# Kernel tuning notes

Measured on AMD Instinct MI355X. Metric: run time of the kernel, lower is better.

Reference implementation:

```python
import jax, jax.numpy as jnp
import numpy as np
import math

B, T, N, D = 8, 4, 2048, 256
M, E = 4096, 8

def setup_inputs() -> dict:
    key = jax.random.key(0)
    ks = jax.random.split(key, 8)
    std = 0.02
    return {
        "prop_embed": jax.random.normal(ks[0], (B, T, N, D), jnp.float32),
        "adap_embed": jax.random.normal(ks[1], (B, N, D), jnp.float32),
        "x_proj_w": jax.random.normal(ks[2], (D, D), jnp.float32) * (1.0 / np.sqrt(D)),
        "x_proj_b": jnp.zeros((D,), jnp.float32),
        "keyMatrix": jax.random.normal(ks[3], (M, D), jnp.float32) * std,
        "memMatrix": jax.random.normal(ks[4], (M, D), jnp.float32) * std,
        "w_gate": jax.random.normal(ks[5], (D, E), jnp.float32) * (1.0 / np.sqrt(D)),
        "w_noise": jax.random.normal(ks[6], (D, E), jnp.float32) * (1.0 / np.sqrt(D)),
    }

def reference(prop_embed, adap_embed, x_proj_w, x_proj_b, keyMatrix, memMatrix, w_gate, w_noise):
    b, t, n, d = prop_embed.shape
    m = memMatrix.shape[0]
    x = jnp.mean(prop_embed, axis=1)                      # [B,N,D]
    q = jnp.tanh(x @ x_proj_w.T + x_proj_b)               # [B,N,D]
    att = jnp.einsum('bnd,md->bnm', q, keyMatrix)         # [B,N,M]
    # eval mode: noise_stddev * self.training == 0, so noisy_logits == clean_logits
    clean_logits = memMatrix @ w_gate                     # [M,E]
    mem_label = jax.nn.softmax(clean_logits, axis=-1)     # [M,E]
    # sparse_qk: keep top-k = int(ln(M)) logits, rest -> -inf
    k = int(math.log(m))
    vals, idx = jax.lax.top_k(att, k)                     # [B,N,k]
    att2 = jnp.full((b * n, m), -jnp.inf, dtype=att.dtype)
    rows = jnp.arange(b * n)[:, None]
    att2 = att2.at[rows, idx.reshape(b * n, k)].set(vals.reshape(b * n, k))
    att_w = jax.nn.softmax(att2, axis=-1).reshape(b, n, m)
    mem_retrieved = jnp.einsum('bnm,md->bnd', att_w, memMatrix)
    label_retrieved = jnp.einsum('bnm,me->bne', att_w, mem_label)
    gate = label_retrieved
    return (gate, mem_retrieved, label_retrieved, mem_label, att_w)
```

## Files before the change

kernel.cpp:

```cpp
#include <hip/hip_runtime.h>
#include <hip/hip_fp16.h>
#include <math.h>

#define Bb 8
#define Tt 4
#define Nn 2048
#define Dd 256
#define Mm 4096
#define Ee 8
#define ROWS (Bb*Nn)
#define KSEL 8
#define KC 16

#define O_GATE 0LL
#define O_MEMR 131072LL
#define O_LABR 4325376LL
#define O_MLAB 4456448LL
#define O_ATTW 4489216LL

#define WS_WT    0LL
#define WS_KH    262144LL
#define WS_CAND  16777216LL
#define WS_QH    150994944LL

typedef float f32x4 __attribute__((ext_vector_type(4)));
typedef short short8 __attribute__((ext_vector_type(8)));
typedef _Float16 f16x8 __attribute__((ext_vector_type(8)));

__device__ __forceinline__ unsigned short f2h(float x) {
    __half h = __float2half(x);
    return *reinterpret_cast<unsigned short*>(&h);
}

__device__ __forceinline__ void gload_lds16(const void* g, void* l) {
    __builtin_amdgcn_global_load_lds(
        (const __attribute__((address_space(1))) unsigned int*)g,
        (__attribute__((address_space(3))) unsigned int*)l,
        16, 0, 0);
}

__global__ __launch_bounds__(256) void k_prep(const float* __restrict__ W, float* __restrict__ WT,
                                              const float* __restrict__ key, unsigned short* __restrict__ kh,
                                              const float* __restrict__ mem, const float* __restrict__ wg,
                                              float* __restrict__ mlab) {
    int b = blockIdx.x, tid = threadIdx.x;
    if (b < 256) {
        int i = b * 256 + tid;
        int r = i >> 8, c = i & 255;
        WT[c * 256 + r] = W[r * 256 + c];
    } else if (b < 256 + 4096) {
        int idx = (b - 256) * 256 + tid;
        kh[idx] = f2h(key[idx]);
    } else {
        int m = (b - 4352) * 256 + tid;
        if (m < Mm) {
            float acc[Ee];
            #pragma unroll
            for (int e = 0; e < Ee; ++e) acc[e] = 0.f;
            const float* mr = mem + (long long)m * Dd;
            for (int d = 0; d < Dd; ++d) {
                float mv = mr[d];
                #pragma unroll
                for (int e = 0; e < Ee; ++e) acc[e] = fmaf(mv, wg[d * Ee + e], acc[e]);
            }
            float mx = acc[0];
            #pragma unroll
            for (int e = 1; e < Ee; ++e) mx = fmaxf(mx, acc[e]);
            float z = 0.f;
            #pragma unroll
            for (int e = 0; e < Ee; ++e) { acc[e] = expf(acc[e] - mx); z += acc[e]; }
            float inv = 1.f / z;
            #pragma unroll
            for (int e = 0; e < Ee; ++e) mlab[(long long)m * Ee + e] = acc[e] * inv;
        }
    }
}

__global__ __launch_bounds__(256) void k_q(const float* __restrict__ prop,
                                           const float* __restrict__ WT,
                                           const float* __restrict__ bias,
                                           float* __restrict__ qf,
                                           unsigned short* __restrict__ qh) {
    __shared__ float xs[16][256];
    int tid = threadIdx.x;
    int row0 = blockIdx.x * 16;
    #pragma unroll
    for (int r = 0; r < 16; ++r) {
        int row = row0 + r;
        int b = row >> 11;
        int n = row & 2047;
        const float* p = prop + ((long long)(b * Tt) * Nn + n) * Dd + tid;
        float s = 0.f;
        #pragma unroll
        for (int t = 0; t < Tt; ++t) s += p[(long long)t * Nn * Dd];
        xs[r][tid] = s * 0.25f;
    }
    __syncthreads();
    float acc[16];
    #pragma unroll
    for (int r = 0; r < 16; ++r) acc[r] = 0.f;
    int c = tid;
    for (int d = 0; d < 256; ++d) {
        float wv = WT[d * 256 + c];
        #pragma unroll
        for (int r = 0; r < 16; ++r) acc[r] = fmaf(xs[r][d], wv, acc[r]);
    }
    float bv = bias[c];
    #pragma unroll
    for (int r = 0; r < 16; ++r) {
        float qv = tanhf(acc[r] + bv);
        long long o = (long long)(row0 + r) * Dd + c;
        qf[o] = qv;
        qh[o] = f2h(qv);
    }
}

__global__ __launch_bounds__(256) void k_att(const unsigned short* __restrict__ qh,
                                             const unsigned short* __restrict__ kh,
                                             unsigned int* __restrict__ cand) {
    __shared__ __align__(16) unsigned short smem[17408];
    int bid = blockIdx.x;
    int swz = (bid & 7) * 512 + (bid >> 3);
    int bx = swz & 31;
    int by = swz >> 5;
    int tid = threadIdx.x;
    int lane = tid & 63, w = tid >> 6;
    int wr = w >> 1, wc = w & 1;
    long long row0 = (long long)by * 128;
    long long col0 = (long long)bx * 128;

    f32x4 acc[4][4];
    #pragma unroll
    for (int m = 0; m < 4; ++m)
        #pragma unroll
        for (int n = 0; n < 4; ++n) acc[m][n] = (f32x4){0.f, 0.f, 0.f, 0.f};

    int rr = lane >> 2;
    int sp = lane & 3;

    auto stage = [&](int k0) {
        #pragma unroll
        for (int t = 0; t < 2; ++t) {
            const unsigned short* src = t ? kh : qh;
            long long b0 = t ? col0 : row0;
            #pragma unroll
            for (int i = 0; i < 2; ++i) {
                int r = w * 32 + i * 16 + rr;
                int sl = sp ^ ((r >> 1) & 3);
                const unsigned short* g = src + (b0 + r) * 256 + k0 * 32 + sl * 8;
                unsigned short* l = smem + t * 4096 + (w * 32 + i * 16) * 32;
                gload_lds16(g, l);
            }
        }
    };

    stage(0);
    for (int k0 = 0; k0 < 8; ++k0) {
        __syncthreads();
        int lr = lane & 15, j = lane >> 4;
        f16x8 ah[4], bh[4];
        #pragma unroll
        for (int m = 0; m < 4; ++m) {
            int r = wr * 64 + m * 16 + lr;
            int off = r * 32 + ((j ^ ((r >> 1) & 3)) * 8);
            ah[m] = *(const f16x8*)(smem + off);
        }
        #pragma unroll
        for (int n = 0; n < 4; ++n) {
            int r = wc * 64 + n * 16 + lr;
            int off = r * 32 + ((j ^ ((r >> 1) & 3)) * 8);
            bh[n] = *(const f16x8*)(smem + 4096 + off);
        }
        #pragma unroll
        for (int m = 0; m < 4; ++m)
            #pragma unroll
            for (int n = 0; n < 4; ++n)
                acc[m][n] = __builtin_amdgcn_mfma_f32_16x16x32_f16(ah[m], bh[n], acc[m][n], 0, 0, 0);
        if (k0 < 7) { __syncthreads(); stage(k0 + 1); }
    }

    __syncthreads();
    {
        int lr = lane & 15, j = lane >> 4;
        #pragma unroll
        for (int m = 0; m < 4; ++m)
            #pragma unroll
            for (int n = 0; n < 4; ++n) {
                int c = wc * 64 + n * 16 + lr;
                #pragma unroll
                for (int reg = 0; reg < 4; ++reg) {
                    int r = wr * 64 + m * 16 + j * 4 + reg;
                    int pc = (((c >> 3) ^ (r & 7)) << 3) | (c & 7);
                    smem[r * 136 + pc] = f2h(acc[m][n][reg]);
                }
            }
    }
    __syncthreads();

    {
        int r2 = tid >> 1;
        int hf = tid & 1;
        unsigned int v[8];
        #pragma unroll
        for (int s = 0; s < 8; ++s) v[s] = 0u;

        #pragma unroll
        for (int t8 = 0; t8 < 8; ++t8) {
            int slot = hf * 8 + t8;
            short8 x8 = *(const short8*)(smem + r2 * 136 + ((slot ^ (r2 & 7)) << 3));
            int gc0 = (int)col0 + slot * 8;
            #pragma unroll
            for (int jj = 0; jj < 8; ++jj) {
                unsigned int b = (unsigned short)x8[jj];
                unsigned int sr = (unsigned)((int)(b << 16) >> 31);
                unsigned int mono = b ^ ((sr >> 17) | 0x8000u);
                unsigned int keyv = (mono << 16) | (unsigned)(4095 - (gc0 + jj));
                if (keyv > v[7]) {
                    unsigned int x = keyv;
                    #pragma unroll
                    for (int s = 0; s < 8; ++s) {
                        unsigned int hi = v[s] > x ? v[s] : x;
                        unsigned int lo = v[s] > x ? x : v[s];
                        v[s] = hi; x = lo;
                    }
                }
            }
        }
        unsigned int nv[8];
        #pragma unroll
        for (int s = 0; s < 8; ++s) {
            unsigned int pv = (unsigned)__shfl_xor((int)v[7 - s], 1);
            nv[s] = v[s] > pv ? v[s] : pv;
        }
        if (hf == 0) {
            unsigned int* dst = cand + ((long long)bx * ROWS + row0 + r2) * 8;
            uint4 a = make_uint4(nv[0], nv[1], nv[2], nv[3]);
            uint4 bq = make_uint4(nv[4], nv[5], nv[6], nv[7]);
            *(uint4*)dst = a;
            *(uint4*)(dst + 4) = bq;
        }
    }
}

__global__ __launch_bounds__(256) void k_final2(const unsigned int* __restrict__ cand,
                                                const float* __restrict__ qf,
                                                const float* __restrict__ key,
                                                const float* __restrict__ mem,
                                                const float* __restrict__ mlab,
                                                float* __restrict__ gate,
                                                float* __restrict__ memr,
                                                float* __restrict__ labr,
                                                float* __restrict__ attw) {
    int tid = threadIdx.x;
    int lane = tid & 63;
    long long row = (long long)blockIdx.x * 4 + (tid >> 6);

    int tl = lane >> 1, of = (lane & 1) * 4;
    uint4 kk = *(const uint4*)(cand + ((long long)tl * ROWS + row) * 8 + of);

    unsigned int v[4];
    #pragma unroll
    for (int s = 0; s < 4; ++s) v[s] = 0u;
    {
        unsigned int ins[4] = {kk.x, kk.y, kk.z, kk.w};
        #pragma unroll
        for (int i = 0; i < 4; ++i) {
            unsigned int x = ins[i];
            #pragma unroll
            for (int s = 0; s < 4; ++s) {
                unsigned int hi = v[s] > x ? v[s] : x;
                unsigned int lo = v[s] > x ? x : v[s];
                v[s] = hi; x = lo;
            }
        }
    }

    unsigned int sk[KC];
    #pragma unroll
    for (int k = 0; k < KC; ++k) {
        unsigned int bv = v[0];
        #pragma unroll
        for (int d = 1; d < 64; d <<= 1) {
            unsigned int ov = (unsigned)__shfl_xor((int)bv, d);
            bv = bv > ov ? bv : ov;
        }
        sk[k] = bv;
        bool won = (v[0] == bv);
        v[0] = won ? v[1] : v[0];
        v[1] = won ? v[2] : v[1];
        v[2] = won ? v[3] : v[2];
        v[3] = won ? 0u : v[3];
    }

    int civ[KC];
    #pragma unroll
    for (int s = 0; s < KC; ++s) civ[s] = 4095 - (int)(sk[s] & 0xFFFu);

    int c = lane & 15, g = lane >> 4;
    int cidx = civ[0];
    #pragma unroll
    for (int s = 1; s < KC; ++s) cidx = (c == s) ? civ[s] : cidx;
    const float* qrow = qf + row * Dd;
    const float* krow = key + (long long)cidx * Dd;
    double dacc = 0.0;
    #pragma unroll
    for (int i = 0; i < 16; ++i) {
        float4 qv = *(const float4*)(qrow + g * 64 + i * 4);
        float4 kv = *(const float4*)(krow + g * 64 + i * 4);
        dacc = fma((double)qv.x, (double)kv.x, dacc);
        dacc = fma((double)qv.y, (double)kv.y, dacc);
        dacc = fma((double)qv.z, (double)kv.z, dacc);
        dacc = fma((double)qv.w, (double)kv.w, dacc);
    }
    dacc += __shfl_xor(dacc, 16);
    dacc += __shfl_xor(dacc, 32);
    float rvf = (float)dacc;

    float cv[KC];
    #pragma unroll
    for (int s = 0; s < KC; ++s) cv[s] = __shfl(rvf, s);

    unsigned int m32[KC];
    #pragma unroll
    for (int s = 0; s < KC; ++s) {
        unsigned int fb = __float_as_uint(cv[s]);
        m32[s] = fb ^ ((unsigned)((int)fb >> 31) | 0x80000000u);
    }
    bool sel[KC];
    #pragma unroll
    for (int s = 0; s < KC; ++s) {
        int r = 0;
        #pragma unroll
        for (int t = 0; t < KC; ++t) {
            if (t != s) {
                bool gt = (m32[t] > m32[s]) || (m32[t] == m32[s] && civ[t] < civ[s]);
                r += gt ? 1 : 0;
            }
        }
        sel[s] = (r < KSEL);
    }

    float mx = cv[0];
    #pragma unroll
    for (int s = 1; s < KC; ++s) mx = fmaxf(mx, cv[s]);
    float p[KC]; float z = 0.f;
    #pragma unroll
    for (int s = 0; s < KC; ++s) { p[s] = sel[s] ? expf(cv[s] - mx) : 0.f; z += p[s]; }
    float inv = 1.f / z;
    #pragma unroll
    for (int s = 0; s < KC; ++s) p[s] *= inv;

    {
        float4 a = make_float4(0.f, 0.f, 0.f, 0.f);
        #pragma unroll
        for (int s = 0; s < KC; ++s) {
            if (sel[s]) {
                const float4 mv = *(const float4*)(mem + (long long)civ[s] * Dd + lane * 4);
                a.x = fmaf(p[s], mv.x, a.x); a.y = fmaf(p[s], mv.y, a.y);
                a.z = fmaf(p[s], mv.z, a.z); a.w = fmaf(p[s], mv.w, a.w);
            }
        }
        *(float4*)(memr + row * Dd + lane * 4) = a;
    }

    if (lane < Ee) {
        float s8 = 0.f;
        #pragma unroll
        for (int s = 0; s < KC; ++s)
            if (sel[s]) s8 = fmaf(p[s], mlab[(long long)civ[s] * Ee + lane], s8);
        gate[row * Ee + lane] = s8;
        labr[row * Ee + lane] = s8;
    }

    float* awrow = attw + row * Mm;
    {
        f32x4 zz = (f32x4){0.f, 0.f, 0.f, 0.f};
        #pragma unroll
        for (int t = 0; t < 16; ++t)
            __builtin_nontemporal_store(zz, (f32x4*)(awrow + (t * 64 + lane) * 4));
    }
    __syncthreads();
    if (lane < KC) {
        float myp = p[0]; int myi = civ[0];
        #pragma unroll
        for (int s = 1; s < KC; ++s) {
            myp = (lane == s) ? p[s] : myp;
            myi = (lane == s) ? civ[s] : myi;
        }
        awrow[myi] = myp;
    }
}

extern "C" void kernel_launch(void* const* d_in, const int* in_sizes, int n_in,
                              void* d_out, int out_size, void* d_ws, size_t ws_size,
                              hipStream_t stream) {
    const float* prop = (const float*)d_in[0];
    const float* W    = (const float*)d_in[2];
    const float* bias = (const float*)d_in[3];
    const float* key  = (const float*)d_in[4];
    const float* mem  = (const float*)d_in[5];
    const float* wg   = (const float*)d_in[6];

    float* out  = (float*)d_out;
    float* gate = out + O_GATE;
    float* memr = out + O_MEMR;
    float* labr = out + O_LABR;
    float* mlab = out + O_MLAB;
    float* attw = out + O_ATTW;

    char* ws = (char*)d_ws;
    float*          WT   = (float*)(ws + WS_WT);
    unsigned short* kh   = (unsigned short*)(ws + WS_KH);
    unsigned int*   cand = (unsigned int*)(ws + WS_CAND);
    unsigned short* qh   = (unsigned short*)(ws + WS_QH);
    float*          qf   = memr;

    k_prep<<<4368, 256, 0, stream>>>(W, WT, key, kh, mem, wg, mlab);
    k_q<<<ROWS / 16, 256, 0, stream>>>(prop, WT, bias, qf, qh);
    k_att<<<4096, 256, 0, stream>>>(qh, kh, cand);
    k_final2<<<ROWS / 4, 256, 0, stream>>>(cand, qf, key, mem, mlab, gate, memr, labr, attw);
}
```

Baseline: 263.6 us.

## Move att_w zero-fill into the attention GEMM kernel and vectorize mean loads

The 268MB zero-fill of the dense attention-weight output moves from the final kernel into the MFMA attention kernel. Each block writes zeros for its own 128x128 tile after the main loop, so the stores can overlap with compute, and the final kernel only scatters the top-k values. The T-mean in k_q now reads float4 instead of scalars. The change relies on kernel launch order so the final scatter runs after the zeros land, and it adds store pressure to the GEMM epilogue.

```diff
diff --git a/kernel.cpp b/kernel.cpp
--- a/kernel.cpp
+++ b/kernel.cpp
@@ -85,15 +85,23 @@
     int tid = threadIdx.x;
     int row0 = blockIdx.x * 16;
     #pragma unroll
-    for (int r = 0; r < 16; ++r) {
+    for (int pass = 0; pass < 4; ++pass) {
+        int r = pass * 4 + (tid >> 6);
+        int d4 = tid & 63;
         int row = row0 + r;
         int b = row >> 11;
         int n = row & 2047;
-        const float* p = prop + ((long long)(b * Tt) * Nn + n) * Dd + tid;
-        float s = 0.f;
-        #pragma unroll
-        for (int t = 0; t < Tt; ++t) s += p[(long long)t * Nn * Dd];
-        xs[r][tid] = s * 0.25f;
+        const float4* p = (const float4*)(prop + ((long long)(b * Tt) * Nn + n) * Dd) + d4;
+        float4 s = make_float4(0.f, 0.f, 0.f, 0.f);
+        #pragma unroll
+        for (int t = 0; t < Tt; ++t) {
+            float4 v = p[(long long)t * Nn * Dd / 4];
+            s.x += v.x; s.y += v.y; s.z += v.z; s.w += v.w;
+        }
+        xs[r][d4 * 4 + 0] = s.x * 0.25f;
+        xs[r][d4 * 4 + 1] = s.y * 0.25f;
+        xs[r][d4 * 4 + 2] = s.z * 0.25f;
+        xs[r][d4 * 4 + 3] = s.w * 0.25f;
     }
     __syncthreads();
     float acc[16];
@@ -117,7 +125,8 @@
 
 __global__ __launch_bounds__(256) void k_att(const unsigned short* __restrict__ qh,
                                              const unsigned short* __restrict__ kh,
-                                             unsigned int* __restrict__ cand) {
+                                             unsigned int* __restrict__ cand,
+                                             float* __restrict__ attw) {
     __shared__ __align__(16) unsigned short smem[17408];
     int bid = blockIdx.x;
     int swz = (bid & 7) * 512 + (bid >> 3);
@@ -177,6 +186,16 @@
             for (int n = 0; n < 4; ++n)
                 acc[m][n] = __builtin_amdgcn_mfma_f32_16x16x32_f16(ah[m], bh[n], acc[m][n], 0, 0, 0);
         if (k0 < 7) { __syncthreads(); stage(k0 + 1); }
+    }
+
+    {
+        f32x4 zz = (f32x4){0.f, 0.f, 0.f, 0.f};
+        #pragma unroll
+        for (int i = 0; i < 16; ++i) {
+            int s = i * 256 + tid;
+            int r = s >> 5, c4 = s & 31;
+            __builtin_nontemporal_store(zz, (f32x4*)(attw + (row0 + r) * Mm + col0 + c4 * 4));
+        }
     }
 
     __syncthreads();
@@ -372,14 +391,6 @@
         labr[row * Ee + lane] = s8;
     }
 
-    float* awrow = attw + row * Mm;
-    {
-        f32x4 zz = (f32x4){0.f, 0.f, 0.f, 0.f};
-        #pragma unroll
-        for (int t = 0; t < 16; ++t)
-            __builtin_nontemporal_store(zz, (f32x4*)(awrow + (t * 64 + lane) * 4));
-    }
-    __syncthreads();
     if (lane < KC) {
         float myp = p[0]; int myi = civ[0];
         #pragma unroll
@@ -387,7 +398,7 @@
             myp = (lane == s) ? p[s] : myp;
             myi = (lane == s) ? civ[s] : myi;
         }
-        awrow[myi] = myp;
+        attw[row * Mm + myi] = myp;
     }
 }
 
@@ -417,6 +428,6 @@
 
     k_prep<<<4368, 256, 0, stream>>>(W, WT, key, kh, mem, wg, mlab);
     k_q<<<ROWS / 16, 256, 0, stream>>>(prop, WT, bias, qf, qh);
-    k_att<<<4096, 256, 0, stream>>>(qh, kh, cand);
+    k_att<<<4096, 256, 0, stream>>>(qh, kh, cand, attw);
     k_final2<<<ROWS / 4, 256, 0, stream>>>(cand, qf, key, mem, mlab, gate, memr, labr, attw);
 }
```

Measured after the change: 248.0 us, median of 2. 1.06x faster.
